# Kernel optimization log

Measured on AMD Instinct MI355X. Metric: run time of the kernel, lower is better.

The kernel has to match this reference:

```python
import jax, jax.numpy as jnp
import numpy as np

B, L, D, K = 32, 4096, 1024, 64


def setup_inputs() -> dict:
    key = jax.random.key(0)
    k1, k2, k3, k4, k5 = jax.random.split(key, 5)
    feats = jax.random.normal(k1, (B, L, D), dtype=jnp.float32)
    assign_w = jax.random.normal(k2, (K, D), dtype=jnp.float32) * (1.0 / np.sqrt(D))
    assign_b = jax.random.normal(k3, (K,), dtype=jnp.float32) * 0.01
    centroids = jax.random.uniform(k4, (K, D), dtype=jnp.float32)
    # ensure at least one valid token per batch row (softmax over L stays finite)
    lens = jax.random.randint(k5, (B,), L // 2, L + 1, dtype=jnp.int32)
    return {"feats": feats, "lens": lens, "assign_w": assign_w,
            "assign_b": assign_b, "centroids": centroids}


def reference(feats, lens, assign_w, assign_b, centroids):
    # feats: (B,L,D); lens: (B,) int; assign_w: (K,D); assign_b: (K,); centroids: (K,D)
    Bq, Lq, Dq = feats.shape
    # padding mask; torch code slices to max(lens) first, but masked positions
    # contribute zero weight after softmax, so keeping full L is equivalent.
    mask = jnp.arange(Lq)[None, :] < lens[:, None]            # (B,L)
    logits = jnp.einsum('bld,kd->blk', feats, assign_w) + assign_b  # (B,L,K)
    logits = jnp.where(mask[:, :, None], logits, -jnp.inf)
    a = jax.nn.softmax(logits, axis=1)                         # softmax over L
    # (a[:,:,:,None] * (feats[:,:,None,:] - centroids)).sum(1) without
    # materializing the (B,L,K,D) residual tensor:
    s = a.sum(axis=1)                                          # (B,K), == 1 analytically
    vlad = jnp.einsum('blk,bld->bkd', a, feats) - s[..., None] * centroids[None]  # (B,K,D)
    out = vlad.min(axis=1)                                     # min over clusters -> (B,D)
    norm = jnp.maximum(jnp.linalg.norm(out, axis=-1, keepdims=True), 1e-12)
    return out / norm
```

## Files before the change

kernel.cpp:

```cpp
#include <hip/hip_runtime.h>
#include <math.h>

#define NB 32
#define NL 4096
#define ND 1024
#define NK 64
#define DTILE 128
#define S_SPLIT 4

typedef __bf16 bf16_t;
typedef __bf16 bf16x8 __attribute__((ext_vector_type(8)));
typedef __bf16 bf16x4 __attribute__((ext_vector_type(4)));
typedef float f32x4_t __attribute__((ext_vector_type(4)));

__global__ __launch_bounds__(256) void k_convw(const float* __restrict__ W,
                                               bf16_t* __restrict__ Wb) {
    const int i = (blockIdx.x * 256 + threadIdx.x) * 4;
    const float4 v = *(const float4*)(W + i);
    bf16x4 o;
    o[0] = (bf16_t)v.x; o[1] = (bf16_t)v.y; o[2] = (bf16_t)v.z; o[3] = (bf16_t)v.w;
    *(bf16x4*)(Wb + i) = o;
}

__global__ __launch_bounds__(256) void k_logits(const float* __restrict__ feats,
                                                const bf16_t* __restrict__ Wb,
                                                const float* __restrict__ bias,
                                                const int* __restrict__ lens,
                                                float* __restrict__ logitsT,
                                                float* __restrict__ pmax,
                                                float* __restrict__ psum) {
    const int bid = blockIdx.x;
    const int b = bid >> 5;
    const int chunk = bid & 31;
    const int l0 = chunk << 7;
    const int len = lens[b];
    if (l0 >= len) return;
    const int t = threadIdx.x;
    const int w = t >> 6;
    const int lane = t & 63;
    const int lr = lane & 15;
    const int oct = lane >> 4;
    const float* fp0 = feats + ((size_t)b * NL + l0 + w * 32 + lr) * ND + oct * 8;
    const float* fp1 = fp0 + (size_t)16 * ND;

    f32x4_t acc[2][4];
#pragma unroll
    for (int m = 0; m < 2; ++m)
#pragma unroll
        for (int j = 0; j < 4; ++j) acc[m][j] = (f32x4_t){0.f, 0.f, 0.f, 0.f};

#pragma unroll 2
    for (int kk = 0; kk < 32; ++kk) {
        const int d = kk * 32;
        const float4 a0 = *(const float4*)(fp0 + d);
        const float4 a1 = *(const float4*)(fp0 + d + 4);
        const float4 a2 = *(const float4*)(fp1 + d);
        const float4 a3 = *(const float4*)(fp1 + d + 4);
        bf16x8 af0, af1;
        af0[0] = (bf16_t)a0.x; af0[1] = (bf16_t)a0.y; af0[2] = (bf16_t)a0.z; af0[3] = (bf16_t)a0.w;
        af0[4] = (bf16_t)a1.x; af0[5] = (bf16_t)a1.y; af0[6] = (bf16_t)a1.z; af0[7] = (bf16_t)a1.w;
        af1[0] = (bf16_t)a2.x; af1[1] = (bf16_t)a2.y; af1[2] = (bf16_t)a2.z; af1[3] = (bf16_t)a2.w;
        af1[4] = (bf16_t)a3.x; af1[5] = (bf16_t)a3.y; af1[6] = (bf16_t)a3.z; af1[7] = (bf16_t)a3.w;
#pragma unroll
        for (int j = 0; j < 4; ++j) {
            const bf16x8 bf = *(const bf16x8*)(Wb + (size_t)(j * 16 + lr) * ND + d + oct * 8);
            acc[0][j] = __builtin_amdgcn_mfma_f32_16x16x32_bf16(af0, bf, acc[0][j], 0, 0, 0);
            acc[1][j] = __builtin_amdgcn_mfma_f32_16x16x32_bf16(af1, bf, acc[1][j], 0, 0, 0);
        }
    }
    float vals[2][4][4];
#pragma unroll
    for (int m = 0; m < 2; ++m)
#pragma unroll
        for (int j = 0; j < 4; ++j) {
            const int k = j * 16 + lr;
            const float bs = bias[k];
#pragma unroll
            for (int r = 0; r < 4; ++r) vals[m][j][r] = acc[m][j][r] + bs;
            const int lb = l0 + w * 32 + m * 16 + oct * 4;
            float4 st = make_float4(vals[m][j][0], vals[m][j][1], vals[m][j][2], vals[m][j][3]);
            *(float4*)(logitsT + ((size_t)b * NK + k) * NL + lb) = st;
        }
    __shared__ float red[64][33];
    __shared__ float bm[64];
    const int slot = w * 8 + oct * 2;
#pragma unroll
    for (int m = 0; m < 2; ++m) {
        const int lbase = l0 + w * 32 + m * 16 + oct * 4;
#pragma unroll
        for (int j = 0; j < 4; ++j) {
            float vm = -1e30f;
#pragma unroll
            for (int r = 0; r < 4; ++r)
                if (lbase + r < len) vm = fmaxf(vm, vals[m][j][r]);
            red[j * 16 + lr][slot + m] = vm;
        }
    }
    __syncthreads();
    if (t < 64) {
        float m = -1e30f;
#pragma unroll
        for (int q = 0; q < 32; ++q) m = fmaxf(m, red[t][q]);
        bm[t] = m;
    }
    __syncthreads();
#pragma unroll
    for (int m = 0; m < 2; ++m) {
        const int lbase = l0 + w * 32 + m * 16 + oct * 4;
#pragma unroll
        for (int j = 0; j < 4; ++j) {
            const float mk = bm[j * 16 + lr];
            float sj = 0.f;
#pragma unroll
            for (int r = 0; r < 4; ++r)
                if (lbase + r < len) sj += __expf(vals[m][j][r] - mk);
            red[j * 16 + lr][slot + m] = sj;
        }
    }
    __syncthreads();
    if (t < 64) {
        float ssum = 0.f;
#pragma unroll
        for (int q = 0; q < 32; ++q) ssum += red[t][q];
        pmax[((size_t)b * 32 + chunk) * 64 + t] = bm[t];
        psum[((size_t)b * 32 + chunk) * 64 + t] = ssum;
    }
}

__global__ void k_sm2(const float* __restrict__ pmax, const float* __restrict__ psum,
                      const int* __restrict__ lens,
                      float* __restrict__ mbuf2) {
    const int b = blockIdx.x;
    const int k = threadIdx.x;
    const int nc = (lens[b] + 127) >> 7;
    float m = -1e30f;
    for (int c = 0; c < nc; ++c) m = fmaxf(m, pmax[((size_t)b * 32 + c) * 64 + k]);
    float s = 0.f;
    for (int c = 0; c < nc; ++c)
        s += psum[((size_t)b * 32 + c) * 64 + k] * __expf(pmax[((size_t)b * 32 + c) * 64 + k] - m);
    mbuf2[b * 64 + k] = m + logf(s);
}

__global__ __launch_bounds__(256, 4) void k_aggregate(const float* __restrict__ feats,
                                                      const float* __restrict__ logitsT,
                                                      const int* __restrict__ lens,
                                                      const float* __restrict__ mbuf2,
                                                      float* __restrict__ pO) {
    const int bid = blockIdx.x;
    const int s  = bid & 3;
    const int dc = (bid >> 2) & 7;
    const int b  = bid >> 5;
    const int d0 = dc * DTILE;
    const int t = threadIdx.x;
    const int w = t >> 6;
    const int lane = t & 63;
    const int lr = lane & 15;
    const int oct = lane >> 4;
    const int len = lens[b];
    const int nT = (len + 63) >> 6;
    const int t0 = (nT * s) >> 2;
    const int t1 = (nT * (s + 1)) >> 2;

    __shared__ char fH[16 * 1024];

    const int kk = w * 16 + lr;
    const float ms2k = mbuf2[b * 64 + kk];
    const float* lgrow = logitsT + ((size_t)b * NK + kk) * NL;

    const int c4 = (t & 31) * 4;
    const int lf0 = (t >> 5) * 4;

    f32x4_t acc[8];
#pragma unroll
    for (int n = 0; n < 8; ++n) acc[n] = (f32x4_t){0.f, 0.f, 0.f, 0.f};

    float4 plg[4];
    float4 pf[2][4];

#define LOADT(tile_)                                                                     \
    {                                                                                    \
        const int lb_ = (tile_) * 64;                                                    \
        plg[0] = *(const float4*)(lgrow + lb_ + oct * 8);                                \
        plg[1] = *(const float4*)(lgrow + lb_ + oct * 8 + 4);                            \
        plg[2] = *(const float4*)(lgrow + lb_ + 32 + oct * 8);                           \
        plg[3] = *(const float4*)(lgrow + lb_ + 32 + oct * 8 + 4);                       \
        _Pragma("unroll")                                                                \
        for (int p_ = 0; p_ < 2; ++p_) {                                                 \
            _Pragma("unroll")                                                            \
            for (int i_ = 0; i_ < 4; ++i_)                                               \
                pf[p_][i_] = *(const float4*)(feats +                                    \
                    ((size_t)b * NL + lb_ + p_ * 32 + lf0 + i_) * ND + d0 + c4);         \
        }                                                                                \
    }

    if (t0 < t1) LOADT(t0);

    for (int tile = t0; tile < t1; ++tile) {
        const int l0 = tile * 64;
        bf16x8 afH[2], afL[2];
#pragma unroll
        for (int ks = 0; ks < 2; ++ks) {
#pragma unroll
            for (int h = 0; h < 2; ++h) {
                const float4 v = plg[ks * 2 + h];
                const int lbase = l0 + ks * 32 + oct * 8 + h * 4;
                float av[4];
                av[0] = (lbase + 0 < len) ? __expf(v.x - ms2k) : 0.f;
                av[1] = (lbase + 1 < len) ? __expf(v.y - ms2k) : 0.f;
                av[2] = (lbase + 2 < len) ? __expf(v.z - ms2k) : 0.f;
                av[3] = (lbase + 3 < len) ? __expf(v.w - ms2k) : 0.f;
#pragma unroll
                for (int c = 0; c < 4; ++c) {
                    const bf16_t hi = (bf16_t)av[c];
                    afH[ks][h * 4 + c] = hi;
                    afL[ks][h * 4 + c] = (bf16_t)(av[c] - (float)hi);
                }
            }
        }
        __syncthreads();
#pragma unroll
        for (int p = 0; p < 2; ++p) {
            const int l4 = p * 32 + lf0;
#pragma unroll
            for (int j = 0; j < 4; ++j) {
                const int d = c4 + j;
                bf16x4 hi;
                hi[0] = (bf16_t)(&pf[p][0].x)[j];
                hi[1] = (bf16_t)(&pf[p][1].x)[j];
                hi[2] = (bf16_t)(&pf[p][2].x)[j];
                hi[3] = (bf16_t)(&pf[p][3].x)[j];
                const int chunk = (l4 >> 3) ^ ((d ^ (d >> 3)) & 7);
                const int off = d * 128 + (chunk << 4) + (l4 & 7) * 2;
                *(bf16x4*)(fH + off) = hi;
            }
        }
        if (tile + 1 < t1) LOADT(tile + 1);
        __syncthreads();
#pragma unroll
        for (int ks = 0; ks < 2; ++ks) {
            const int cbase = ks * 4 + oct;
#pragma unroll
            for (int n = 0; n < 8; ++n) {
                const int d = n * 16 + lr;
                const int foff = d * 128 + ((cbase ^ ((d ^ (d >> 3)) & 7)) << 4);
                const bf16x8 bfH = *(const bf16x8*)(fH + foff);
                acc[n] = __builtin_amdgcn_mfma_f32_16x16x32_bf16(afH[ks], bfH, acc[n], 0, 0, 0);
                acc[n] = __builtin_amdgcn_mfma_f32_16x16x32_bf16(afL[ks], bfH, acc[n], 0, 0, 0);
            }
        }
    }
#undef LOADT
    float* po = pO + ((size_t)((b * 8 + dc) * S_SPLIT + s)) * (NK * DTILE);
#pragma unroll
    for (int n = 0; n < 8; ++n) {
#pragma unroll
        for (int r = 0; r < 4; ++r) {
            const int k = w * 16 + oct * 4 + r;
            po[k * DTILE + n * 16 + lr] = acc[n][r];
        }
    }
}

__global__ __launch_bounds__(128) void k_combine(const float* __restrict__ pO,
                                                 const float* __restrict__ centroids,
                                                 float* __restrict__ outun) {
    const int b = blockIdx.x >> 3;
    const int d = (blockIdx.x & 7) * 128 + threadIdx.x;
    const int dc = d >> 7;
    const int dl = d & 127;
    const float* base = pO + ((size_t)(b * 8 + dc)) * S_SPLIT * NK * DTILE;
    float mn = 1e30f;
    for (int k = 0; k < NK; ++k) {
        float v = 0.f;
#pragma unroll
        for (int s = 0; s < S_SPLIT; ++s) v += base[(size_t)(s * NK + k) * DTILE + dl];
        v -= centroids[(size_t)k * ND + d];
        mn = fminf(mn, v);
    }
    outun[(size_t)b * ND + d] = mn;
}

__global__ __launch_bounds__(256) void k_norm(const float* __restrict__ outun,
                                              float* __restrict__ out) {
    const int b = blockIdx.x;
    const int t = threadIdx.x;
    float ss = 0.f;
    for (int d = t; d < ND; d += 256) {
        const float v = outun[(size_t)b * ND + d];
        ss += v * v;
    }
#pragma unroll
    for (int off = 32; off > 0; off >>= 1) ss += __shfl_down(ss, off);
    __shared__ float red[4];
    if ((t & 63) == 0) red[t >> 6] = ss;
    __syncthreads();
    const float tot = red[0] + red[1] + red[2] + red[3];
    const float inv = 1.0f / fmaxf(sqrtf(tot), 1e-12f);
    for (int d = t; d < ND; d += 256) out[(size_t)b * ND + d] = outun[(size_t)b * ND + d] * inv;
}

extern "C" void kernel_launch(void* const* d_in, const int* in_sizes, int n_in,
                              void* d_out, int out_size, void* d_ws, size_t ws_size,
                              hipStream_t stream) {
    const float* feats     = (const float*)d_in[0];
    const int*   lens      = (const int*)d_in[1];
    const float* W         = (const float*)d_in[2];
    const float* bias      = (const float*)d_in[3];
    const float* centroids = (const float*)d_in[4];
    float* out = (float*)d_out;

    char* ws = (char*)d_ws;
    size_t off = 0;
    bf16_t* Wb     = (bf16_t*)(ws + off); off += (size_t)NK * ND * sizeof(bf16_t);
    float* logitsT = (float*)(ws + off);  off += (size_t)NB * NL * NK * sizeof(float);
    float* pmax    = (float*)(ws + off);  off += (size_t)NB * 32 * NK * sizeof(float);
    float* psum    = (float*)(ws + off);  off += (size_t)NB * 32 * NK * sizeof(float);
    float* mbuf2   = (float*)(ws + off);  off += (size_t)NB * NK * sizeof(float);
    float* outun   = (float*)(ws + off);  off += (size_t)NB * ND * sizeof(float);
    float* pO      = (float*)(ws + off);

    k_convw<<<NK * ND / 1024, 256, 0, stream>>>(W, Wb);
    k_logits<<<NB * (NL / 128), 256, 0, stream>>>(feats, Wb, bias, lens, logitsT, pmax, psum);
    k_sm2<<<NB, 64, 0, stream>>>(pmax, psum, lens, mbuf2);
    k_aggregate<<<NB * 8 * S_SPLIT, 256, 0, stream>>>(feats, logitsT, lens, mbuf2, pO);
    k_combine<<<NB * 8, 128, 0, stream>>>(pO, centroids, outun);
    k_norm<<<NB, 256, 0, stream>>>(outun, out);
}
```

Measured before the change: 284.6 us.

## Enlarge per-warp register tiles in logits and aggregate MFMA kernels

k_logits now gives each block 256 tokens, and each warp computes 64 rows with 4x4 MFMA accumulators. This reuses every W fragment load across four row tiles and halves the number of blocks and partial softmax stats. k_aggregate changes its warp mapping so each warp covers 32 clusters by 64 feature columns instead of 16 by 128. This cuts the shared-memory B-fragment reads per MFMA and loads the logits directly inside the loop instead of prefetching them. The cost is more register pressure, with the aggregate occupancy hint lowered from 4 to 3 and logits set to 2, and fewer blocks for the logits grid.

```diff
diff --git a/kernel.cpp b/kernel.cpp
--- a/kernel.cpp
+++ b/kernel.cpp
@@ -22,17 +22,17 @@
     *(bf16x4*)(Wb + i) = o;
 }
 
-__global__ __launch_bounds__(256) void k_logits(const float* __restrict__ feats,
-                                                const bf16_t* __restrict__ Wb,
-                                                const float* __restrict__ bias,
-                                                const int* __restrict__ lens,
-                                                float* __restrict__ logitsT,
-                                                float* __restrict__ pmax,
-                                                float* __restrict__ psum) {
+__global__ __launch_bounds__(256, 2) void k_logits(const float* __restrict__ feats,
+                                                   const bf16_t* __restrict__ Wb,
+                                                   const float* __restrict__ bias,
+                                                   const int* __restrict__ lens,
+                                                   float* __restrict__ logitsT,
+                                                   float* __restrict__ pmax,
+                                                   float* __restrict__ psum) {
     const int bid = blockIdx.x;
-    const int b = bid >> 5;
-    const int chunk = bid & 31;
-    const int l0 = chunk << 7;
+    const int b = bid >> 4;
+    const int chunk = bid & 15;
+    const int l0 = chunk << 8;
     const int len = lens[b];
     if (l0 >= len) return;
     const int t = threadIdx.x;
@@ -40,90 +40,92 @@
     const int lane = t & 63;
     const int lr = lane & 15;
     const int oct = lane >> 4;
-    const float* fp0 = feats + ((size_t)b * NL + l0 + w * 32 + lr) * ND + oct * 8;
-    const float* fp1 = fp0 + (size_t)16 * ND;
-
-    f32x4_t acc[2][4];
-#pragma unroll
-    for (int m = 0; m < 2; ++m)
+    const int lw = l0 + w * 64;
+    const float* fp = feats + ((size_t)b * NL + lw + lr) * ND + oct * 8;
+
+    f32x4_t acc[4][4];
+#pragma unroll
+    for (int m = 0; m < 4; ++m)
 #pragma unroll
         for (int j = 0; j < 4; ++j) acc[m][j] = (f32x4_t){0.f, 0.f, 0.f, 0.f};
 
 #pragma unroll 2
     for (int kk = 0; kk < 32; ++kk) {
         const int d = kk * 32;
-        const float4 a0 = *(const float4*)(fp0 + d);
-        const float4 a1 = *(const float4*)(fp0 + d + 4);
-        const float4 a2 = *(const float4*)(fp1 + d);
-        const float4 a3 = *(const float4*)(fp1 + d + 4);
-        bf16x8 af0, af1;
-        af0[0] = (bf16_t)a0.x; af0[1] = (bf16_t)a0.y; af0[2] = (bf16_t)a0.z; af0[3] = (bf16_t)a0.w;
-        af0[4] = (bf16_t)a1.x; af0[5] = (bf16_t)a1.y; af0[6] = (bf16_t)a1.z; af0[7] = (bf16_t)a1.w;
-        af1[0] = (bf16_t)a2.x; af1[1] = (bf16_t)a2.y; af1[2] = (bf16_t)a2.z; af1[3] = (bf16_t)a2.w;
-        af1[4] = (bf16_t)a3.x; af1[5] = (bf16_t)a3.y; af1[6] = (bf16_t)a3.z; af1[7] = (bf16_t)a3.w;
+        bf16x8 af[4];
+#pragma unroll
+        for (int mt = 0; mt < 4; ++mt) {
+            const float4 a0 = *(const float4*)(fp + (size_t)mt * 16 * ND + d);
+            const float4 a1 = *(const float4*)(fp + (size_t)mt * 16 * ND + d + 4);
+            af[mt][0] = (bf16_t)a0.x; af[mt][1] = (bf16_t)a0.y;
+            af[mt][2] = (bf16_t)a0.z; af[mt][3] = (bf16_t)a0.w;
+            af[mt][4] = (bf16_t)a1.x; af[mt][5] = (bf16_t)a1.y;
+            af[mt][6] = (bf16_t)a1.z; af[mt][7] = (bf16_t)a1.w;
+        }
 #pragma unroll
         for (int j = 0; j < 4; ++j) {
             const bf16x8 bf = *(const bf16x8*)(Wb + (size_t)(j * 16 + lr) * ND + d + oct * 8);
-            acc[0][j] = __builtin_amdgcn_mfma_f32_16x16x32_bf16(af0, bf, acc[0][j], 0, 0, 0);
-            acc[1][j] = __builtin_amdgcn_mfma_f32_16x16x32_bf16(af1, bf, acc[1][j], 0, 0, 0);
-        }
-    }
-    float vals[2][4][4];
-#pragma unroll
-    for (int m = 0; m < 2; ++m)
+#pragma unroll
+            for (int mt = 0; mt < 4; ++mt)
+                acc[mt][j] = __builtin_amdgcn_mfma_f32_16x16x32_bf16(af[mt], bf, acc[mt][j], 0, 0, 0);
+        }
+    }
+    float vals[4][4][4];
+#pragma unroll
+    for (int mt = 0; mt < 4; ++mt)
 #pragma unroll
         for (int j = 0; j < 4; ++j) {
             const int k = j * 16 + lr;
             const float bs = bias[k];
 #pragma unroll
-            for (int r = 0; r < 4; ++r) vals[m][j][r] = acc[m][j][r] + bs;
-            const int lb = l0 + w * 32 + m * 16 + oct * 4;
-            float4 st = make_float4(vals[m][j][0], vals[m][j][1], vals[m][j][2], vals[m][j][3]);
+            for (int r = 0; r < 4; ++r) vals[mt][j][r] = acc[mt][j][r] + bs;
+            const int lb = lw + mt * 16 + oct * 4;
+            float4 st = make_float4(vals[mt][j][0], vals[mt][j][1], vals[mt][j][2], vals[mt][j][3]);
             *(float4*)(logitsT + ((size_t)b * NK + k) * NL + lb) = st;
         }
-    __shared__ float red[64][33];
+    __shared__ float red[64][17];
     __shared__ float bm[64];
-    const int slot = w * 8 + oct * 2;
-#pragma unroll
-    for (int m = 0; m < 2; ++m) {
-        const int lbase = l0 + w * 32 + m * 16 + oct * 4;
-#pragma unroll
-        for (int j = 0; j < 4; ++j) {
-            float vm = -1e30f;
+    const int slot = w * 4 + oct;
+#pragma unroll
+    for (int j = 0; j < 4; ++j) {
+        float vm = -1e30f;
+#pragma unroll
+        for (int mt = 0; mt < 4; ++mt) {
+            const int lbase = lw + mt * 16 + oct * 4;
 #pragma unroll
             for (int r = 0; r < 4; ++r)
-                if (lbase + r < len) vm = fmaxf(vm, vals[m][j][r]);
-            red[j * 16 + lr][slot + m] = vm;
-        }
+                if (lbase + r < len) vm = fmaxf(vm, vals[mt][j][r]);
+        }
+        red[j * 16 + lr][slot] = vm;
     }
     __syncthreads();
     if (t < 64) {
         float m = -1e30f;
 #pragma unroll
-        for (int q = 0; q < 32; ++q) m = fmaxf(m, red[t][q]);
+        for (int q = 0; q < 16; ++q) m = fmaxf(m, red[t][q]);
         bm[t] = m;
     }
     __syncthreads();
 #pragma unroll
-    for (int m = 0; m < 2; ++m) {
-        const int lbase = l0 + w * 32 + m * 16 + oct * 4;
-#pragma unroll
-        for (int j = 0; j < 4; ++j) {
-            const float mk = bm[j * 16 + lr];
-            float sj = 0.f;
+    for (int j = 0; j < 4; ++j) {
+        const float mk = bm[j * 16 + lr];
+        float sj = 0.f;
+#pragma unroll
+        for (int mt = 0; mt < 4; ++mt) {
+            const int lbase = lw + mt * 16 + oct * 4;
 #pragma unroll
             for (int r = 0; r < 4; ++r)
-                if (lbase + r < len) sj += __expf(vals[m][j][r] - mk);
-            red[j * 16 + lr][slot + m] = sj;
-        }
+                if (lbase + r < len) sj += __expf(vals[mt][j][r] - mk);
+        }
+        red[j * 16 + lr][slot] = sj;
     }
     __syncthreads();
     if (t < 64) {
         float ssum = 0.f;
 #pragma unroll
-        for (int q = 0; q < 32; ++q) ssum += red[t][q];
-        pmax[((size_t)b * 32 + chunk) * 64 + t] = bm[t];
-        psum[((size_t)b * 32 + chunk) * 64 + t] = ssum;
+        for (int q = 0; q < 16; ++q) ssum += red[t][q];
+        pmax[((size_t)b * 16 + chunk) * 64 + t] = bm[t];
+        psum[((size_t)b * 16 + chunk) * 64 + t] = ssum;
     }
 }
 
@@ -132,16 +134,16 @@
                       float* __restrict__ mbuf2) {
     const int b = blockIdx.x;
     const int k = threadIdx.x;
-    const int nc = (lens[b] + 127) >> 7;
+    const int nc = (lens[b] + 255) >> 8;
     float m = -1e30f;
-    for (int c = 0; c < nc; ++c) m = fmaxf(m, pmax[((size_t)b * 32 + c) * 64 + k]);
+    for (int c = 0; c < nc; ++c) m = fmaxf(m, pmax[((size_t)b * 16 + c) * 64 + k]);
     float s = 0.f;
     for (int c = 0; c < nc; ++c)
-        s += psum[((size_t)b * 32 + c) * 64 + k] * __expf(pmax[((size_t)b * 32 + c) * 64 + k] - m);
+        s += psum[((size_t)b * 16 + c) * 64 + k] * __expf(pmax[((size_t)b * 16 + c) * 64 + k] - m);
     mbuf2[b * 64 + k] = m + logf(s);
 }
 
-__global__ __launch_bounds__(256, 4) void k_aggregate(const float* __restrict__ feats,
+__global__ __launch_bounds__(256, 3) void k_aggregate(const float* __restrict__ feats,
                                                       const float* __restrict__ logitsT,
                                                       const int* __restrict__ lens,
                                                       const float* __restrict__ mbuf2,
@@ -152,7 +154,8 @@
     const int b  = bid >> 5;
     const int d0 = dc * DTILE;
     const int t = threadIdx.x;
-    const int w = t >> 6;
+    const int kh = (t >> 6) & 1;
+    const int dh = t >> 7;
     const int lane = t & 63;
     const int lr = lane & 15;
     const int oct = lane >> 4;
@@ -163,27 +166,26 @@
 
     __shared__ char fH[16 * 1024];
 
-    const int kk = w * 16 + lr;
-    const float ms2k = mbuf2[b * 64 + kk];
-    const float* lgrow = logitsT + ((size_t)b * NK + kk) * NL;
+    const int kk0 = kh * 32 + lr;
+    const float ms0 = mbuf2[b * 64 + kk0];
+    const float ms1 = mbuf2[b * 64 + kk0 + 16];
+    const float* lg0 = logitsT + ((size_t)b * NK + kk0) * NL;
+    const float* lg1 = lg0 + (size_t)16 * NL;
 
     const int c4 = (t & 31) * 4;
     const int lf0 = (t >> 5) * 4;
 
-    f32x4_t acc[8];
-#pragma unroll
-    for (int n = 0; n < 8; ++n) acc[n] = (f32x4_t){0.f, 0.f, 0.f, 0.f};
-
-    float4 plg[4];
+    f32x4_t acc[2][4];
+#pragma unroll
+    for (int m = 0; m < 2; ++m)
+#pragma unroll
+        for (int n = 0; n < 4; ++n) acc[m][n] = (f32x4_t){0.f, 0.f, 0.f, 0.f};
+
     float4 pf[2][4];
 
-#define LOADT(tile_)                                                                     \
+#define LOADF(tile_)                                                                     \
     {                                                                                    \
         const int lb_ = (tile_) * 64;                                                    \
-        plg[0] = *(const float4*)(lgrow + lb_ + oct * 8);                                \
-        plg[1] = *(const float4*)(lgrow + lb_ + oct * 8 + 4);                            \
-        plg[2] = *(const float4*)(lgrow + lb_ + 32 + oct * 8);                           \
-        plg[3] = *(const float4*)(lgrow + lb_ + 32 + oct * 8 + 4);                       \
         _Pragma("unroll")                                                                \
         for (int p_ = 0; p_ < 2; ++p_) {                                                 \
             _Pragma("unroll")                                                            \
@@ -193,27 +195,37 @@
         }                                                                                \
     }
 
-    if (t0 < t1) LOADT(t0);
+    if (t0 < t1) LOADF(t0);
 
     for (int tile = t0; tile < t1; ++tile) {
         const int l0 = tile * 64;
-        bf16x8 afH[2], afL[2];
-#pragma unroll
-        for (int ks = 0; ks < 2; ++ks) {
-#pragma unroll
-            for (int h = 0; h < 2; ++h) {
-                const float4 v = plg[ks * 2 + h];
-                const int lbase = l0 + ks * 32 + oct * 8 + h * 4;
-                float av[4];
-                av[0] = (lbase + 0 < len) ? __expf(v.x - ms2k) : 0.f;
-                av[1] = (lbase + 1 < len) ? __expf(v.y - ms2k) : 0.f;
-                av[2] = (lbase + 2 < len) ? __expf(v.z - ms2k) : 0.f;
-                av[3] = (lbase + 3 < len) ? __expf(v.w - ms2k) : 0.f;
-#pragma unroll
-                for (int c = 0; c < 4; ++c) {
-                    const bf16_t hi = (bf16_t)av[c];
-                    afH[ks][h * 4 + c] = hi;
-                    afL[ks][h * 4 + c] = (bf16_t)(av[c] - (float)hi);
+        bf16x8 afH[2][2], afL[2][2];
+#pragma unroll
+        for (int mt = 0; mt < 2; ++mt) {
+            const float* lg = mt ? lg1 : lg0;
+            const float msk = mt ? ms1 : ms0;
+            float4 g[4];
+            g[0] = *(const float4*)(lg + l0 + oct * 8);
+            g[1] = *(const float4*)(lg + l0 + oct * 8 + 4);
+            g[2] = *(const float4*)(lg + l0 + 32 + oct * 8);
+            g[3] = *(const float4*)(lg + l0 + 32 + oct * 8 + 4);
+#pragma unroll
+            for (int ks = 0; ks < 2; ++ks) {
+#pragma unroll
+                for (int h = 0; h < 2; ++h) {
+                    const float4 v = g[ks * 2 + h];
+                    const int lbase = l0 + ks * 32 + oct * 8 + h * 4;
+                    float av[4];
+                    av[0] = (lbase + 0 < len) ? __expf(v.x - msk) : 0.f;
+                    av[1] = (lbase + 1 < len) ? __expf(v.y - msk) : 0.f;
+                    av[2] = (lbase + 2 < len) ? __expf(v.z - msk) : 0.f;
+                    av[3] = (lbase + 3 < len) ? __expf(v.w - msk) : 0.f;
+#pragma unroll
+                    for (int c = 0; c < 4; ++c) {
+                        const bf16_t hi = (bf16_t)av[c];
+                        afH[mt][ks][h * 4 + c] = hi;
+                        afL[mt][ks][h * 4 + c] = (bf16_t)(av[c] - (float)hi);
+                    }
                 }
             }
         }
@@ -234,31 +246,39 @@
                 *(bf16x4*)(fH + off) = hi;
             }
         }
-        if (tile + 1 < t1) LOADT(tile + 1);
+        if (tile + 1 < t1) LOADF(tile + 1);
         __syncthreads();
 #pragma unroll
         for (int ks = 0; ks < 2; ++ks) {
             const int cbase = ks * 4 + oct;
-#pragma unroll
-            for (int n = 0; n < 8; ++n) {
-                const int d = n * 16 + lr;
+            bf16x8 bfv[4];
+#pragma unroll
+            for (int n = 0; n < 4; ++n) {
+                const int d = dh * 64 + n * 16 + lr;
                 const int foff = d * 128 + ((cbase ^ ((d ^ (d >> 3)) & 7)) << 4);
-                const bf16x8 bfH = *(const bf16x8*)(fH + foff);
-                acc[n] = __builtin_amdgcn_mfma_f32_16x16x32_bf16(afH[ks], bfH, acc[n], 0, 0, 0);
-                acc[n] = __builtin_amdgcn_mfma_f32_16x16x32_bf16(afL[ks], bfH, acc[n], 0, 0, 0);
+                bfv[n] = *(const bf16x8*)(fH + foff);
             }
-        }
-    }
-#undef LOADT
+#pragma unroll
+            for (int mt = 0; mt < 2; ++mt)
+#pragma unroll
+                for (int n = 0; n < 4; ++n) {
+                    acc[mt][n] = __builtin_amdgcn_mfma_f32_16x16x32_bf16(afH[mt][ks], bfv[n], acc[mt][n], 0, 0, 0);
+                    acc[mt][n] = __builtin_amdgcn_mfma_f32_16x16x32_bf16(afL[mt][ks], bfv[n], acc[mt][n], 0, 0, 0);
+                }
+        }
+    }
+#undef LOADF
     float* po = pO + ((size_t)((b * 8 + dc) * S_SPLIT + s)) * (NK * DTILE);
 #pragma unroll
-    for (int n = 0; n < 8; ++n) {
-#pragma unroll
-        for (int r = 0; r < 4; ++r) {
-            const int k = w * 16 + oct * 4 + r;
-            po[k * DTILE + n * 16 + lr] = acc[n][r];
-        }
-    }
+    for (int mt = 0; mt < 2; ++mt)
+#pragma unroll
+        for (int n = 0; n < 4; ++n) {
+#pragma unroll
+            for (int r = 0; r < 4; ++r) {
+                const int k = kh * 32 + mt * 16 + oct * 4 + r;
+                po[k * DTILE + dh * 64 + n * 16 + lr] = acc[mt][n][r];
+            }
+        }
 }
 
 __global__ __launch_bounds__(128) void k_combine(const float* __restrict__ pO,
@@ -313,14 +333,14 @@
     size_t off = 0;
     bf16_t* Wb     = (bf16_t*)(ws + off); off += (size_t)NK * ND * sizeof(bf16_t);
     float* logitsT = (float*)(ws + off);  off += (size_t)NB * NL * NK * sizeof(float);
-    float* pmax    = (float*)(ws + off);  off += (size_t)NB * 32 * NK * sizeof(float);
-    float* psum    = (float*)(ws + off);  off += (size_t)NB * 32 * NK * sizeof(float);
+    float* pmax    = (float*)(ws + off);  off += (size_t)NB * 16 * NK * sizeof(float);
+    float* psum    = (float*)(ws + off);  off += (size_t)NB * 16 * NK * sizeof(float);
     float* mbuf2   = (float*)(ws + off);  off += (size_t)NB * NK * sizeof(float);
     float* outun   = (float*)(ws + off);  off += (size_t)NB * ND * sizeof(float);
     float* pO      = (float*)(ws + off);
 
     k_convw<<<NK * ND / 1024, 256, 0, stream>>>(W, Wb);
-    k_logits<<<NB * (NL / 128), 256, 0, stream>>>(feats, Wb, bias, lens, logitsT, pmax, psum);
+    k_logits<<<NB * (NL / 256), 256, 0, stream>>>(feats, Wb, bias, lens, logitsT, pmax, psum);
     k_sm2<<<NB, 64, 0, stream>>>(pmax, psum, lens, mbuf2);
     k_aggregate<<<NB * 8 * S_SPLIT, 256, 0, stream>>>(feats, logitsT, lens, mbuf2, pO);
     k_combine<<<NB * 8, 128, 0, stream>>>(pO, centroids, outun);
```

New measurement: 281.8 us (median of 2 runs). No clear change (-1.0%).

## Retile aggregate warps to 2x4 MFMA blocks and double sequence split

Applied to the files above, without the earlier changes.

Each wave in the aggregation kernel now computes a 32-cluster by 64-column tile instead of a 16-cluster by 128-column tile. This halves the LDS B-fragment reads per MFMA and reuses each loaded feature fragment across two cluster tiles. The sequence split doubles from 4 to 8, giving twice as many blocks for better occupancy, but it doubles the partial output written to pO and read back in combine. Launch bounds are relaxed, and logits loads move from prefetch to in-loop loads, which may expose latency.

```diff
diff --git a/kernel.cpp b/kernel.cpp
--- a/kernel.cpp
+++ b/kernel.cpp
@@ -6,7 +6,7 @@
 #define ND 1024
 #define NK 64
 #define DTILE 128
-#define S_SPLIT 4
+#define S_SPLIT 8
 
 typedef __bf16 bf16_t;
 typedef __bf16 bf16x8 __attribute__((ext_vector_type(8)));
@@ -22,13 +22,13 @@
     *(bf16x4*)(Wb + i) = o;
 }
 
-__global__ __launch_bounds__(256) void k_logits(const float* __restrict__ feats,
-                                                const bf16_t* __restrict__ Wb,
-                                                const float* __restrict__ bias,
-                                                const int* __restrict__ lens,
-                                                float* __restrict__ logitsT,
-                                                float* __restrict__ pmax,
-                                                float* __restrict__ psum) {
+__global__ __launch_bounds__(256, 2) void k_logits(const float* __restrict__ feats,
+                                                   const bf16_t* __restrict__ Wb,
+                                                   const float* __restrict__ bias,
+                                                   const int* __restrict__ lens,
+                                                   float* __restrict__ logitsT,
+                                                   float* __restrict__ pmax,
+                                                   float* __restrict__ psum) {
     const int bid = blockIdx.x;
     const int b = bid >> 5;
     const int chunk = bid & 31;
@@ -141,49 +141,49 @@
     mbuf2[b * 64 + k] = m + logf(s);
 }
 
-__global__ __launch_bounds__(256, 4) void k_aggregate(const float* __restrict__ feats,
+__global__ __launch_bounds__(256, 3) void k_aggregate(const float* __restrict__ feats,
                                                       const float* __restrict__ logitsT,
                                                       const int* __restrict__ lens,
                                                       const float* __restrict__ mbuf2,
                                                       float* __restrict__ pO) {
     const int bid = blockIdx.x;
-    const int s  = bid & 3;
-    const int dc = (bid >> 2) & 7;
-    const int b  = bid >> 5;
+    const int s  = bid & 7;
+    const int dc = (bid >> 3) & 7;
+    const int b  = bid >> 6;
     const int d0 = dc * DTILE;
     const int t = threadIdx.x;
-    const int w = t >> 6;
+    const int kh = (t >> 6) & 1;
+    const int dh = t >> 7;
     const int lane = t & 63;
     const int lr = lane & 15;
     const int oct = lane >> 4;
     const int len = lens[b];
     const int nT = (len + 63) >> 6;
-    const int t0 = (nT * s) >> 2;
-    const int t1 = (nT * (s + 1)) >> 2;
+    const int t0 = (nT * s) >> 3;
+    const int t1 = (nT * (s + 1)) >> 3;
 
     __shared__ char fH[16 * 1024];
 
-    const int kk = w * 16 + lr;
-    const float ms2k = mbuf2[b * 64 + kk];
-    const float* lgrow = logitsT + ((size_t)b * NK + kk) * NL;
+    const int kk0 = kh * 32 + lr;
+    const float ms0 = mbuf2[b * 64 + kk0];
+    const float ms1 = mbuf2[b * 64 + kk0 + 16];
+    const float* lg0 = logitsT + ((size_t)b * NK + kk0) * NL;
+    const float* lg1 = lg0 + (size_t)16 * NL;
 
     const int c4 = (t & 31) * 4;
     const int lf0 = (t >> 5) * 4;
 
-    f32x4_t acc[8];
-#pragma unroll
-    for (int n = 0; n < 8; ++n) acc[n] = (f32x4_t){0.f, 0.f, 0.f, 0.f};
-
-    float4 plg[4];
+    f32x4_t acc[2][4];
+#pragma unroll
+    for (int m = 0; m < 2; ++m)
+#pragma unroll
+        for (int n = 0; n < 4; ++n) acc[m][n] = (f32x4_t){0.f, 0.f, 0.f, 0.f};
+
     float4 pf[2][4];
 
-#define LOADT(tile_)                                                                     \
+#define LOADF(tile_)                                                                     \
     {                                                                                    \
         const int lb_ = (tile_) * 64;                                                    \
-        plg[0] = *(const float4*)(lgrow + lb_ + oct * 8);                                \
-        plg[1] = *(const float4*)(lgrow + lb_ + oct * 8 + 4);                            \
-        plg[2] = *(const float4*)(lgrow + lb_ + 32 + oct * 8);                           \
-        plg[3] = *(const float4*)(lgrow + lb_ + 32 + oct * 8 + 4);                       \
         _Pragma("unroll")                                                                \
         for (int p_ = 0; p_ < 2; ++p_) {                                                 \
             _Pragma("unroll")                                                            \
@@ -193,27 +193,37 @@
         }                                                                                \
     }
 
-    if (t0 < t1) LOADT(t0);
+    if (t0 < t1) LOADF(t0);
 
     for (int tile = t0; tile < t1; ++tile) {
         const int l0 = tile * 64;
-        bf16x8 afH[2], afL[2];
-#pragma unroll
-        for (int ks = 0; ks < 2; ++ks) {
-#pragma unroll
-            for (int h = 0; h < 2; ++h) {
-                const float4 v = plg[ks * 2 + h];
-                const int lbase = l0 + ks * 32 + oct * 8 + h * 4;
-                float av[4];
-                av[0] = (lbase + 0 < len) ? __expf(v.x - ms2k) : 0.f;
-                av[1] = (lbase + 1 < len) ? __expf(v.y - ms2k) : 0.f;
-                av[2] = (lbase + 2 < len) ? __expf(v.z - ms2k) : 0.f;
-                av[3] = (lbase + 3 < len) ? __expf(v.w - ms2k) : 0.f;
-#pragma unroll
-                for (int c = 0; c < 4; ++c) {
-                    const bf16_t hi = (bf16_t)av[c];
-                    afH[ks][h * 4 + c] = hi;
-                    afL[ks][h * 4 + c] = (bf16_t)(av[c] - (float)hi);
+        bf16x8 afH[2][2], afL[2][2];
+#pragma unroll
+        for (int mt = 0; mt < 2; ++mt) {
+            const float* lg = mt ? lg1 : lg0;
+            const float msk = mt ? ms1 : ms0;
+            float4 g[4];
+            g[0] = *(const float4*)(lg + l0 + oct * 8);
+            g[1] = *(const float4*)(lg + l0 + oct * 8 + 4);
+            g[2] = *(const float4*)(lg + l0 + 32 + oct * 8);
+            g[3] = *(const float4*)(lg + l0 + 32 + oct * 8 + 4);
+#pragma unroll
+            for (int ks = 0; ks < 2; ++ks) {
+#pragma unroll
+                for (int h = 0; h < 2; ++h) {
+                    const float4 v = g[ks * 2 + h];
+                    const int lbase = l0 + ks * 32 + oct * 8 + h * 4;
+                    float av[4];
+                    av[0] = (lbase + 0 < len) ? __expf(v.x - msk) : 0.f;
+                    av[1] = (lbase + 1 < len) ? __expf(v.y - msk) : 0.f;
+                    av[2] = (lbase + 2 < len) ? __expf(v.z - msk) : 0.f;
+                    av[3] = (lbase + 3 < len) ? __expf(v.w - msk) : 0.f;
+#pragma unroll
+                    for (int c = 0; c < 4; ++c) {
+                        const bf16_t hi = (bf16_t)av[c];
+                        afH[mt][ks][h * 4 + c] = hi;
+                        afL[mt][ks][h * 4 + c] = (bf16_t)(av[c] - (float)hi);
+                    }
                 }
             }
         }
@@ -234,31 +244,39 @@
                 *(bf16x4*)(fH + off) = hi;
             }
         }
-        if (tile + 1 < t1) LOADT(tile + 1);
+        if (tile + 1 < t1) LOADF(tile + 1);
         __syncthreads();
 #pragma unroll
         for (int ks = 0; ks < 2; ++ks) {
             const int cbase = ks * 4 + oct;
-#pragma unroll
-            for (int n = 0; n < 8; ++n) {
-                const int d = n * 16 + lr;
+            bf16x8 bfv[4];
+#pragma unroll
+            for (int n = 0; n < 4; ++n) {
+                const int d = dh * 64 + n * 16 + lr;
                 const int foff = d * 128 + ((cbase ^ ((d ^ (d >> 3)) & 7)) << 4);
-                const bf16x8 bfH = *(const bf16x8*)(fH + foff);
-                acc[n] = __builtin_amdgcn_mfma_f32_16x16x32_bf16(afH[ks], bfH, acc[n], 0, 0, 0);
-                acc[n] = __builtin_amdgcn_mfma_f32_16x16x32_bf16(afL[ks], bfH, acc[n], 0, 0, 0);
+                bfv[n] = *(const bf16x8*)(fH + foff);
             }
-        }
-    }
-#undef LOADT
+#pragma unroll
+            for (int mt = 0; mt < 2; ++mt)
+#pragma unroll
+                for (int n = 0; n < 4; ++n) {
+                    acc[mt][n] = __builtin_amdgcn_mfma_f32_16x16x32_bf16(afH[mt][ks], bfv[n], acc[mt][n], 0, 0, 0);
+                    acc[mt][n] = __builtin_amdgcn_mfma_f32_16x16x32_bf16(afL[mt][ks], bfv[n], acc[mt][n], 0, 0, 0);
+                }
+        }
+    }
+#undef LOADF
     float* po = pO + ((size_t)((b * 8 + dc) * S_SPLIT + s)) * (NK * DTILE);
 #pragma unroll
-    for (int n = 0; n < 8; ++n) {
-#pragma unroll
-        for (int r = 0; r < 4; ++r) {
-            const int k = w * 16 + oct * 4 + r;
-            po[k * DTILE + n * 16 + lr] = acc[n][r];
-        }
-    }
+    for (int mt = 0; mt < 2; ++mt)
+#pragma unroll
+        for (int n = 0; n < 4; ++n) {
+#pragma unroll
+            for (int r = 0; r < 4; ++r) {
+                const int k = kh * 32 + mt * 16 + oct * 4 + r;
+                po[k * DTILE + dh * 64 + n * 16 + lr] = acc[mt][n][r];
+            }
+        }
 }
 
 __global__ __launch_bounds__(128) void k_combine(const float* __restrict__ pO,
```

Measured after the change: 287.7 us. No clear change (+1.1%).
